# Performance work log

Hardware: AMD Instinct MI355X
Metric: run time of the kernel (lower is better)

Reference implementation:

```python
import jax, jax.numpy as jnp
import numpy as np

B, N, DIM, H, DH = 1, 2048, 1024, 16, 64


def setup_inputs() -> dict:
    key = jax.random.key(0)
    k1, k2, k3 = jax.random.split(key, 3)
    x = jax.random.normal(k1, (B, N, DIM), dtype=jnp.float32)
    # LinearNoBias(dim, 6*heads*dim_head): weight [6*H*DH, DIM]
    w_qkv = jax.random.normal(k2, (6 * H * DH, DIM), dtype=jnp.float32) * (DIM ** -0.5)
    # LinearNoBias(heads*dim_head, dim): weight [DIM, H*DH]
    w_out = jax.random.normal(k3, (DIM, H * DH), dtype=jnp.float32) * ((H * DH) ** -0.5)
    return {"x": x, "w_qkv": w_qkv, "w_out": w_out}


def reference(x, w_qkv, w_out):
    b, n, _ = x.shape
    scale = DH ** -0.5
    qkvs = x @ w_qkv.T  # [b, n, 6*H*DH]
    # rearrange 'b n (qkv h d) -> qkv b h n d'
    qkvs = qkvs.reshape(b, n, 6, H, DH).transpose(2, 0, 3, 1, 4)
    qu, ku, vu, qc, kc, vc = qkvs
    qu = qu * scale
    qc = qc * scale

    upper = jnp.triu(jnp.ones((n, n), dtype=bool), 1)  # strict upper triangle

    # term1: causal (lower-incl-diag) qc . vu
    term1 = jnp.einsum('bhid,bhjd->bhij', qc, vu)
    term1 = jnp.where(upper, 0.0, term1)

    # sigmoid lookahead term: strict-upper only
    sig = jax.nn.sigmoid(jnp.einsum('bhid,bhjd->bhij', qu, ku))
    sig = jnp.where(upper, sig, 0.0)

    Su = jnp.einsum('bhij,bhkj->bhik', term1, sig)

    Sc = jnp.einsum('bhid,bhjd->bhij', qc, kc)
    neg = -jnp.finfo(Sc.dtype).max
    Sc = jnp.where(upper, neg, Sc)

    scores = Sc - jax.nn.silu(Su)
    attn = jax.nn.softmax(scores, axis=-1)
    out = jnp.einsum('bhij,bhjd->bhid', attn, vc)  # [b,h,n,d]
    out = out.transpose(0, 2, 1, 3).reshape(b, n, H * DH)
    return out @ w_out.T
```

## Files before the change

kernel.cpp:

```cpp
#include <hip/hip_runtime.h>

using f16 = _Float16;
using half8  = __attribute__((ext_vector_type(8))) f16;
using half4v = __attribute__((ext_vector_type(4))) f16;
using float4v = __attribute__((ext_vector_type(4))) float;

#define DEV static __device__ __forceinline__

constexpr int N = 2048, DIM = 1024, H = 16, DH = 64, F6 = 6144;
constexpr int LDSH = 136;
constexpr int TS = 128 * 128;
constexpr int NTILES = 136;
constexpr int KD = 2048 * 64;

DEV int PL(int i, int k) { return i * (i + 1) / 2 + k; }
DEV int PU(int a, int b) { return a * 16 - a * (a - 1) / 2 + (b - a); }

template<int ROWS, int THREADS>
DEV void stage64(const f16* __restrict__ g, int strideHalves, f16* lds, int tid) {
#pragma unroll
  for (int q = 0; q < (ROWS * 8) / THREADS; ++q) {
    const int chunk = q * THREADS + tid;
    const int m = chunk >> 3, c = (chunk & 7) ^ (m & 7);
    const f16* gp = g + (size_t)m * strideHalves + c * 8;
    __builtin_amdgcn_global_load_lds(
        (const __attribute__((address_space(1))) unsigned int*)gp,
        (__attribute__((address_space(3))) unsigned int*)(lds + chunk * 8), 16, 0, 0);
  }
}

DEV half8 rdfrag(const f16* T, int m, int ks, int q) {
  const int c = (ks * 4 + q) ^ (m & 7);
  return *(const half8*)(T + m * 64 + c * 8);
}

DEV void wfrag(f16* T, int row, int col, f16 v) {
  T[row * 64 + ((((col >> 3) ^ (row & 7)) << 3) | (col & 7))] = v;
}

DEV void gemm64(const f16* As, const f16* Bs, int wm, int wn, int l, float4v acc[4][4]) {
  const int q = l >> 4, mm = l & 15;
#pragma unroll
  for (int ks = 0; ks < 2; ++ks) {
    half8 af[4], bf[4];
#pragma unroll
    for (int mi = 0; mi < 4; ++mi) af[mi] = rdfrag(As, wm + mm + mi * 16, ks, q);
#pragma unroll
    for (int ni = 0; ni < 4; ++ni) bf[ni] = rdfrag(Bs, wn + mm + ni * 16, ks, q);
#pragma unroll
    for (int mi = 0; mi < 4; ++mi)
#pragma unroll
      for (int ni = 0; ni < 4; ++ni)
        acc[mi][ni] = __builtin_amdgcn_mfma_f32_16x16x32_f16(af[mi], bf[ni], acc[mi][ni], 0, 0, 0);
  }
}

DEV void decode_pair(int p, int& ti, int& tk) {
  int t = (int)((sqrtf(8.f * p + 1.f) - 1.f) * 0.5f);
  while (t * (t + 1) / 2 > p) --t;
  while ((t + 1) * (t + 2) / 2 <= p) ++t;
  const int i2 = p - t * (t + 1) / 2;
  ti = (15 - t) + i2;
  tk = i2;
}

__global__ __launch_bounds__(256) void k_cast(const float* __restrict__ s, f16* __restrict__ d, int n4) {
  int i = blockIdx.x * 256 + threadIdx.x;
  if (i < n4) {
    float4 v = ((const float4*)s)[i];
    half4v h;
    h[0] = (f16)v.x; h[1] = (f16)v.y; h[2] = (f16)v.z; h[3] = (f16)v.w;
    ((half4v*)d)[i] = h;
  }
}

__global__ __launch_bounds__(256) void k_qkv(const f16* __restrict__ xh, const f16* __restrict__ wh,
                                             f16* __restrict__ quh, f16* __restrict__ kuh,
                                             f16* __restrict__ vuh, f16* __restrict__ qch,
                                             f16* __restrict__ kch, f16* __restrict__ vcT,
                                             f16* __restrict__ vuT) {
  __shared__ __align__(16) f16 lds[128 * LDSH];
  f16* As = lds; f16* Bs = lds + 128 * 64;
  const int tid = threadIdx.x, w = tid >> 6, l = tid & 63;
  const int tm = blockIdx.x * 128, tf = blockIdx.y * 128;
  const int wm = (w >> 1) * 64, wn = (w & 1) * 64;
  float4v acc[4][4] = {};
  for (int k0 = 0; k0 < DIM; k0 += 64) {
    stage64<128, 256>(xh + (size_t)tm * DIM + k0, DIM, As, tid);
    stage64<128, 256>(wh + (size_t)tf * DIM + k0, DIM, Bs, tid);
    __syncthreads();
    gemm64(As, Bs, wm, wn, l, acc);
    __syncthreads();
  }
  const int rbase = (l >> 4) * 4, cidx = l & 15;
  const int t = tf >> 10;
  const float sc = (t == 0 || t == 3) ? 0.125f : 1.f;
  if (t == 5 || t == 2) {
    f16* T = (t == 5) ? vcT : vuT;
#pragma unroll
    for (int mi = 0; mi < 4; ++mi)
#pragma unroll
      for (int ni = 0; ni < 4; ++ni) {
        const int f = tf + wn + ni * 16 + cidx;
        const int h = (f & 1023) >> 6, d = f & 63;
        half4v p;
#pragma unroll
        for (int r = 0; r < 4; ++r) p[r] = (f16)acc[mi][ni][r];
        *(half4v*)(T + ((size_t)h * DH + d) * N + (tm + wm + mi * 16 + rbase)) = p;
      }
  }
  if (t != 5) {
#pragma unroll
    for (int mi = 0; mi < 4; ++mi)
#pragma unroll
      for (int ni = 0; ni < 4; ++ni)
#pragma unroll
        for (int r = 0; r < 4; ++r)
          lds[(wm + mi * 16 + rbase + r) * LDSH + wn + ni * 16 + cidx] = (f16)(acc[mi][ni][r] * sc);
    __syncthreads();
    f16* dst = (t == 0) ? quh : (t == 1) ? kuh : (t == 2) ? vuh : (t == 3) ? qch : kch;
    const int hb = (tf & 1023) >> 6;
#pragma unroll
    for (int q = 0; q < 8; ++q) {
      const int idx = q * 256 + tid, row = idx >> 4, c = idx & 15;
      const int h = hb + (c >> 3), d0 = (c & 7) * 8, n = tm + row;
      *(half8*)(dst + ((size_t)h * N + n) * DH + d0) = *(const half8*)(lds + row * LDSH + c * 8);
    }
  }
}

__global__ __launch_bounds__(256) void k_dsig(const f16* __restrict__ quh, const f16* __restrict__ kuh,
                                              const f16* __restrict__ qch, const f16* __restrict__ vuh,
                                              const f16* __restrict__ vuT,
                                              f16* __restrict__ sigb, f16* __restrict__ DC,
                                              f16* __restrict__ diagb, int h0) {
  __shared__ __align__(16) f16 L[32768];
  f16* quA = L; f16* kuB = L + 8192; f16* s1 = L + 16384; f16* s2 = L + 24576;
  int b, a;
  decode_pair(blockIdx.y, b, a);
  const int hl = blockIdx.x, h = h0 + hl;
  const int tid = threadIdx.x, w = tid >> 6, l = tid & 63;
  const int q = l >> 4, m = l & 15;
  const int wm = (w >> 1) * 64, wn = (w & 1) * 64;
  const size_t ho = (size_t)h * N * DH;

  stage64<128, 256>(quh + ho + (size_t)(a * 128) * DH, DH, quA, tid);
  stage64<128, 256>(kuh + ho + (size_t)(b * 128) * DH, DH, kuB, tid);
  __syncthreads();
  float4v acc[4][4] = {};
  gemm64(quA, kuB, wm, wn, l, acc);
  __syncthreads();
  stage64<64, 256>(vuT + (size_t)h * DH * N + b * 128, N, kuB, tid);
  stage64<64, 256>(vuT + (size_t)h * DH * N + b * 128 + 64, N, kuB + 4096, tid);
#pragma unroll
  for (int mi = 0; mi < 4; ++mi)
#pragma unroll
    for (int ni = 0; ni < 4; ++ni)
#pragma unroll
      for (int r = 0; r < 4; ++r) {
        const int row = wm + mi * 16 + q * 4 + r;
        const int col = wn + ni * 16 + m;
        const float x = acc[mi][ni][r];
        const f16 sv = (b * 128 + col > a * 128 + row) ? (f16)(1.f / (1.f + __expf(-x))) : (f16)0.f;
        wfrag((col < 64) ? s1 : s2, row, col & 63, sv);
      }
  __syncthreads();
  {
    f16* Sg = sigb + ((size_t)hl * NTILES + PU(a, b)) * TS;
#pragma unroll
    for (int qq = 0; qq < 8; ++qq) {
      const int idx = qq * 256 + tid, row = idx >> 4, c = idx & 15;
      const f16* p = ((c >> 3) ? s2 : s1) + row * 64 + (((c & 7) ^ (row & 7)) << 3);
      *(half8*)(Sg + (size_t)row * 128 + c * 8) = *(const half8*)p;
    }
  }
  float4v dacc[2][4] = {};
#pragma unroll
  for (int p = 0; p < 2; ++p)
#pragma unroll
    for (int ks = 0; ks < 2; ++ks) {
      half8 bf[4], af[2];
#pragma unroll
      for (int ni = 0; ni < 4; ++ni) bf[ni] = rdfrag(kuB + p * 4096, ni * 16 + m, ks, q);
#pragma unroll
      for (int mi = 0; mi < 2; ++mi) af[mi] = rdfrag(p ? s2 : s1, w * 32 + mi * 16 + m, ks, q);
#pragma unroll
      for (int mi = 0; mi < 2; ++mi)
#pragma unroll
        for (int ni = 0; ni < 4; ++ni)
          dacc[mi][ni] = __builtin_amdgcn_mfma_f32_16x16x32_f16(af[mi], bf[ni], dacc[mi][ni], 0, 0, 0);
    }
  __syncthreads();
  if (a == b) {
    stage64<128, 256>(qch + ho + (size_t)(a * 128) * DH, DH, quA, tid);
    stage64<128, 256>(vuh + ho + (size_t)(a * 128) * DH, DH, kuB, tid);
  }
  {
    f16* epsD = s1;
#pragma unroll
    for (int mi = 0; mi < 2; ++mi)
#pragma unroll
      for (int ni = 0; ni < 4; ++ni)
#pragma unroll
        for (int r = 0; r < 4; ++r)
          epsD[(w * 32 + mi * 16 + q * 4 + r) * 68 + ni * 16 + m] = (f16)dacc[mi][ni][r];
    __syncthreads();
    f16* Dg = DC + ((size_t)hl * 16 + b) * KD + (size_t)(a * 128) * 64;
#pragma unroll
    for (int qq = 0; qq < 4; ++qq) {
      const int idx = qq * 256 + tid, row = idx >> 3, c = idx & 7;
      *(half8*)(Dg + (size_t)row * 64 + c * 8) = *(const half8*)(epsD + row * 68 + c * 8);
    }
  }
  if (a == b) {
    float4v tacc[4][4] = {};
    gemm64(quA, kuB, wm, wn, l, tacc);
    f16* Tg = diagb + ((size_t)hl * 16 + a) * TS;
#pragma unroll
    for (int mi = 0; mi < 4; ++mi)
#pragma unroll
      for (int ni = 0; ni < 4; ++ni)
#pragma unroll
        for (int r = 0; r < 4; ++r) {
          const int row = wm + mi * 16 + q * 4 + r, col = wn + ni * 16 + m;
          Tg[(size_t)row * 128 + col] = (col <= row) ? (f16)tacc[mi][ni][r] : (f16)0.f;
        }
  }
}

__global__ __launch_bounds__(256) void k_scan(f16* __restrict__ DC, int total) {
  const int idx = blockIdx.x * 256 + threadIdx.x;
  if (idx >= total) return;
  const int g = idx >> 17, off = idx & (KD - 1);
  const int a = off >> 13;
  f16* p = DC + (size_t)g * 16 * KD + off;
  float s = 0.f;
#pragma unroll
  for (int T = 0; T < 16; ++T) {
    const float v = (T >= a) ? (float)p[(size_t)T * KD] : 0.f;
    p[(size_t)T * KD] = (f16)s;
    s += v;
  }
}

__global__ __launch_bounds__(256) void k_favs(const f16* __restrict__ qch, const f16* __restrict__ kch,
                                              const f16* __restrict__ DC, const f16* __restrict__ sigb,
                                              const f16* __restrict__ diagb, const f16* __restrict__ vcT,
                                              f16* __restrict__ Oh, int h0) {
  __shared__ float mlds[4][32], llds[4][32];
  __shared__ __align__(16) float olds[32][68];
  __shared__ __align__(16) f16 plds[4][32 * 64];
  const int hl = blockIdx.x, h = h0 + hl;
  const int mt = 63 - (int)blockIdx.y;
  const int tid = threadIdx.x, w = tid >> 6, l = tid & 63;
  const int q = l >> 4, m = l & 15;
  const int ti = mt >> 2, r0 = mt * 32;
  const size_t ho = (size_t)h * N * DH;
  const f16* qc = qch + ho;
  const f16* kc = kch + ho;
  const f16* Cb = DC + ((size_t)hl * 16 + ti) * KD;
  const f16* Td = diagb + ((size_t)hl * 16 + ti) * TS;
  const f16* Sgb = sigb + (size_t)hl * NTILES * TS;
  const f16* V = vcT + (size_t)h * DH * N;
  f16* pw = plds[w];

  half8 qcA[2][2], tdA[2][4];
  const int dr = (mt & 3) * 32;
#pragma unroll
  for (int mi = 0; mi < 2; ++mi) {
#pragma unroll
    for (int ks = 0; ks < 2; ++ks)
      qcA[mi][ks] = *(const half8*)(qc + (size_t)(r0 + mi * 16 + m) * DH + ks * 32 + q * 8);
#pragma unroll
    for (int ks = 0; ks < 4; ++ks)
      tdA[mi][ks] = *(const half8*)(Td + (size_t)(dr + mi * 16 + m) * 128 + ks * 32 + q * 8);
  }

  float4v o[2][4] = {};
  float mrun[2][4], lrun[2][4];
#pragma unroll
  for (int mi = 0; mi < 2; ++mi)
#pragma unroll
    for (int r = 0; r < 4; ++r) { mrun[mi][r] = -1e30f; lrun[mi][r] = 0.f; }

  const int jtmax = mt >> 1;
  for (int jt = w; jt <= jtmax; jt += 4) {
    const int k0 = jt * 64;
    const int tkt = jt >> 1, koff = (jt & 1) * 64;
    const f16* Sg = Sgb + (size_t)PU(tkt, ti) * TS;
    float4v s[2][4] = {};
#pragma unroll
    for (int ks = 0; ks < 2; ++ks) {
      half8 bf[4];
#pragma unroll
      for (int ni = 0; ni < 4; ++ni)
        bf[ni] = *(const half8*)(Cb + (size_t)(k0 + ni * 16 + m) * 64 + ks * 32 + q * 8);
#pragma unroll
      for (int mi = 0; mi < 2; ++mi)
#pragma unroll
        for (int ni = 0; ni < 4; ++ni)
          s[mi][ni] = __builtin_amdgcn_mfma_f32_16x16x32_f16(qcA[mi][ks], bf[ni], s[mi][ni], 0, 0, 0);
    }
#pragma unroll
    for (int ks = 0; ks < 4; ++ks) {
      half8 bf[4];
#pragma unroll
      for (int ni = 0; ni < 4; ++ni)
        bf[ni] = *(const half8*)(Sg + (size_t)(koff + ni * 16 + m) * 128 + ks * 32 + q * 8);
#pragma unroll
      for (int mi = 0; mi < 2; ++mi)
#pragma unroll
        for (int ni = 0; ni < 4; ++ni)
          s[mi][ni] = __builtin_amdgcn_mfma_f32_16x16x32_f16(tdA[mi][ks], bf[ni], s[mi][ni], 0, 0, 0);
    }
#pragma unroll
    for (int mi = 0; mi < 2; ++mi)
#pragma unroll
      for (int ni = 0; ni < 4; ++ni)
#pragma unroll
        for (int r = 0; r < 4; ++r) {
          const float x = s[mi][ni][r];
          s[mi][ni][r] = -(x / (1.f + __expf(-x)));
        }
#pragma unroll
    for (int ks = 0; ks < 2; ++ks) {
      half8 bf[4];
#pragma unroll
      for (int ni = 0; ni < 4; ++ni)
        bf[ni] = *(const half8*)(kc + (size_t)(k0 + ni * 16 + m) * DH + ks * 32 + q * 8);
#pragma unroll
      for (int mi = 0; mi < 2; ++mi)
#pragma unroll
        for (int ni = 0; ni < 4; ++ni)
          s[mi][ni] = __builtin_amdgcn_mfma_f32_16x16x32_f16(qcA[mi][ks], bf[ni], s[mi][ni], 0, 0, 0);
    }
    if (jt == jtmax) {
#pragma unroll
      for (int mi = 0; mi < 2; ++mi)
#pragma unroll
        for (int ni = 0; ni < 4; ++ni) {
          const int col = k0 + ni * 16 + m;
#pragma unroll
          for (int r = 0; r < 4; ++r)
            if (col > r0 + mi * 16 + q * 4 + r) s[mi][ni][r] = -1e30f;
        }
    }
    float al[2][4], ts[2][4];
#pragma unroll
    for (int mi = 0; mi < 2; ++mi)
#pragma unroll
      for (int r = 0; r < 4; ++r) {
        float tmx = fmaxf(fmaxf(s[mi][0][r], s[mi][1][r]), fmaxf(s[mi][2][r], s[mi][3][r]));
#pragma unroll
        for (int x = 1; x < 16; x <<= 1) tmx = fmaxf(tmx, __shfl_xor(tmx, x));
        const float nm = fmaxf(mrun[mi][r], tmx);
        al[mi][r] = __expf(mrun[mi][r] - nm);
        mrun[mi][r] = nm;
        ts[mi][r] = 0.f;
      }
#pragma unroll
    for (int mi = 0; mi < 2; ++mi)
#pragma unroll
      for (int ni = 0; ni < 4; ++ni)
#pragma unroll
        for (int r = 0; r < 4; ++r) {
          const float p = __expf(s[mi][ni][r] - mrun[mi][r]);
          wfrag(pw, mi * 16 + q * 4 + r, ni * 16 + m, (f16)p);
          ts[mi][r] += p;
        }
#pragma unroll
    for (int mi = 0; mi < 2; ++mi)
#pragma unroll
      for (int r = 0; r < 4; ++r) {
#pragma unroll
        for (int x = 1; x < 16; x <<= 1) ts[mi][r] += __shfl_xor(ts[mi][r], x);
        lrun[mi][r] = lrun[mi][r] * al[mi][r] + ts[mi][r];
#pragma unroll
        for (int ni = 0; ni < 4; ++ni) o[mi][ni][r] *= al[mi][r];
      }
#pragma unroll
    for (int ks = 0; ks < 2; ++ks) {
      half8 af[2], bf[4];
#pragma unroll
      for (int mi = 0; mi < 2; ++mi) af[mi] = rdfrag(pw, mi * 16 + m, ks, q);
#pragma unroll
      for (int ni = 0; ni < 4; ++ni)
        bf[ni] = *(const half8*)(V + (size_t)(ni * 16 + m) * N + k0 + ks * 32 + q * 8);
#pragma unroll
      for (int mi = 0; mi < 2; ++mi)
#pragma unroll
        for (int ni = 0; ni < 4; ++ni)
          o[mi][ni] = __builtin_amdgcn_mfma_f32_16x16x32_f16(af[mi], bf[ni], o[mi][ni], 0, 0, 0);
    }
  }
  if (m == 0)
#pragma unroll
    for (int mi = 0; mi < 2; ++mi)
#pragma unroll
      for (int r = 0; r < 4; ++r) {
        mlds[w][mi * 16 + q * 4 + r] = mrun[mi][r];
        llds[w][mi * 16 + q * 4 + r] = lrun[mi][r];
      }
  __syncthreads();
#pragma unroll
  for (int mi = 0; mi < 2; ++mi)
#pragma unroll
    for (int r = 0; r < 4; ++r) {
      const int row = mi * 16 + q * 4 + r;
      const float mstar = fmaxf(fmaxf(mlds[0][row], mlds[1][row]), fmaxf(mlds[2][row], mlds[3][row]));
      const float sw = __expf(mlds[w][row] - mstar);
#pragma unroll
      for (int ni = 0; ni < 4; ++ni) o[mi][ni][r] *= sw;
    }
#pragma unroll
  for (int t = 0; t < 4; ++t) {
    if (w == t) {
#pragma unroll
      for (int mi = 0; mi < 2; ++mi)
#pragma unroll
        for (int ni = 0; ni < 4; ++ni)
#pragma unroll
          for (int r = 0; r < 4; ++r) {
            const int row = mi * 16 + q * 4 + r, col = ni * 16 + m;
            if (t == 0) olds[row][col] = o[mi][ni][r];
            else olds[row][col] += o[mi][ni][r];
          }
    }
    __syncthreads();
  }
  const int row = tid >> 3, c = tid & 7;
  const float mstar = fmaxf(fmaxf(mlds[0][row], mlds[1][row]), fmaxf(mlds[2][row], mlds[3][row]));
  float denom = 0.f;
#pragma unroll
  for (int t = 0; t < 4; ++t) denom += __expf(mlds[t][row] - mstar) * llds[t][row];
  const float inv = 1.f / denom;
  half8 o8;
#pragma unroll
  for (int e = 0; e < 8; ++e) o8[e] = (f16)(olds[row][c * 8 + e] * inv);
  *(half8*)(Oh + (size_t)(mt * 32 + row) * (H * DH) + h * DH + c * 8) = o8;
}

__global__ __launch_bounds__(256) void k_out(const f16* __restrict__ Oh, const f16* __restrict__ wo,
                                             float* __restrict__ out) {
  __shared__ __align__(16) f16 lds[128 * LDSH];
  f16* As = lds; f16* Bs = lds + 128 * 64;
  const int tid = threadIdx.x, w = tid >> 6, l = tid & 63;
  const int tm = blockIdx.x * 128, tn = blockIdx.y * 128;
  const int wm = (w >> 1) * 64, wn = (w & 1) * 64;
  float4v acc[4][4] = {};
  for (int k0 = 0; k0 < DIM; k0 += 64) {
    stage64<128, 256>(Oh + (size_t)tm * DIM + k0, DIM, As, tid);
    stage64<128, 256>(wo + (size_t)tn * DIM + k0, DIM, Bs, tid);
    __syncthreads();
    gemm64(As, Bs, wm, wn, l, acc);
    __syncthreads();
  }
  const int rbase = (l >> 4) * 4, cidx = l & 15;
#pragma unroll
  for (int mi = 0; mi < 4; ++mi)
#pragma unroll
    for (int ni = 0; ni < 4; ++ni)
#pragma unroll
      for (int r = 0; r < 4; ++r) {
        const int n = tm + wm + mi * 16 + rbase + r;
        const int dmo = tn + wn + ni * 16 + cidx;
        out[(size_t)n * DIM + dmo] = acc[mi][ni][r];
      }
}

extern "C" void kernel_launch(void* const* d_in, const int* in_sizes, int n_in,
                              void* d_out, int out_size, void* d_ws, size_t ws_size,
                              hipStream_t stream) {
  const float* x = (const float*)d_in[0];
  const float* wqkv = (const float*)d_in[1];
  const float* wout = (const float*)d_in[2];
  float* out = (float*)d_out;
  char* ws = (char*)d_ws;

  size_t off = 0;
  auto alloc = [&](size_t b) { size_t o = off; off += (b + 255) & ~(size_t)255; return o; };
  f16* xh  = (f16*)(ws + alloc((size_t)N * DIM * 2));
  f16* wqh = (f16*)(ws + alloc((size_t)F6 * DIM * 2));
  f16* woh = (f16*)(ws + alloc((size_t)DIM * H * DH * 2));
  f16* quh = (f16*)(ws + alloc((size_t)H * N * DH * 2));
  f16* kuh = (f16*)(ws + alloc((size_t)H * N * DH * 2));
  f16* vuh = (f16*)(ws + alloc((size_t)H * N * DH * 2));
  f16* qch = (f16*)(ws + alloc((size_t)H * N * DH * 2));
  f16* kch = (f16*)(ws + alloc((size_t)H * N * DH * 2));
  f16* vcT = (f16*)(ws + alloc((size_t)H * DH * N * 2));
  f16* vuT = (f16*)(ws + alloc((size_t)H * DH * N * 2));
  f16* Oh  = (f16*)(ws + alloc((size_t)N * H * DH * 2));
  const size_t persist = off;

  const size_t per_head = ((size_t)NTILES * TS + (size_t)16 * KD + (size_t)16 * TS) * 2;
  int G = (ws_size > persist + 4096) ? (int)((ws_size - persist - 4096) / per_head) : 1;
  if (G < 1) G = 1;
  if (G > 16) G = 16;
  {
    const int R = (H + G - 1) / G;
    G = (H + R - 1) / R;
  }
  f16* sigb  = (f16*)(ws + alloc((size_t)G * NTILES * TS * 2));
  f16* DC    = (f16*)(ws + alloc((size_t)G * 16 * KD * 2));
  f16* diagb = (f16*)(ws + alloc((size_t)G * 16 * TS * 2));

  k_cast<<<(N * DIM / 4 + 255) / 256, 256, 0, stream>>>(x, xh, N * DIM / 4);
  k_cast<<<(F6 * DIM / 4 + 255) / 256, 256, 0, stream>>>(wqkv, wqh, F6 * DIM / 4);
  k_cast<<<(DIM * H * DH / 4 + 255) / 256, 256, 0, stream>>>(wout, woh, DIM * H * DH / 4);

  k_qkv<<<dim3(N / 128, F6 / 128), 256, 0, stream>>>(xh, wqh, quh, kuh, vuh, qch, kch, vcT, vuT);

  for (int h0 = 0; h0 < H; h0 += G) {
    const int Gr = (H - h0 < G) ? (H - h0) : G;
    k_dsig<<<dim3(Gr, 136), 256, 0, stream>>>(quh, kuh, qch, vuh, vuT, sigb, DC, diagb, h0);
    k_scan<<<(Gr * KD + 255) / 256, 256, 0, stream>>>(DC, Gr * KD);
    k_favs<<<dim3(Gr, 64), 256, 0, stream>>>(qch, kch, DC, sigb, diagb, vcT, Oh, h0);
  }

  k_out<<<dim3(16, 8), 256, 0, stream>>>(Oh, woh, out);
}
```

Baseline: 323.1 us.

## Prefetch B-fragments ahead of MFMAs and interleave block-row order in k_favs

The inner loop of k_favs now issues the global loads for the C, K, sigmoid and V fragments early, into registers, so that their latency overlaps earlier MFMA chains instead of stalling each k-step. The block-to-row-tile mapping also changes from strictly descending to alternating long and short causal rows, which changes how work is spread over time across CUs. This raises register pressure (about 48 extra half8 values held live), which could cut occupancy or cause spills.

```diff
diff --git a/kernel.cpp b/kernel.cpp
--- a/kernel.cpp
+++ b/kernel.cpp
@@ -251,7 +251,8 @@
   __shared__ __align__(16) float olds[32][68];
   __shared__ __align__(16) f16 plds[4][32 * 64];
   const int hl = blockIdx.x, h = h0 + hl;
-  const int mt = 63 - (int)blockIdx.y;
+  const int y = (int)blockIdx.y;
+  const int mt = (y < 32) ? (63 - 2 * y) : (2 * (y - 32));
   const int tid = threadIdx.x, w = tid >> 6, l = tid & 63;
   const int q = l >> 4, m = l & 15;
   const int ti = mt >> 2, r0 = mt * 32;
@@ -288,31 +289,56 @@
     const int k0 = jt * 64;
     const int tkt = jt >> 1, koff = (jt & 1) * 64;
     const f16* Sg = Sgb + (size_t)PU(tkt, ti) * TS;
+    half8 bC[2][4], bK[2][4], bS0[2][4];
+#pragma unroll
+    for (int ks = 0; ks < 2; ++ks)
+#pragma unroll
+      for (int ni = 0; ni < 4; ++ni)
+        bC[ks][ni] = *(const half8*)(Cb + (size_t)(k0 + ni * 16 + m) * 64 + ks * 32 + q * 8);
+#pragma unroll
+    for (int ks = 0; ks < 2; ++ks)
+#pragma unroll
+      for (int ni = 0; ni < 4; ++ni)
+        bK[ks][ni] = *(const half8*)(kc + (size_t)(k0 + ni * 16 + m) * DH + ks * 32 + q * 8);
+#pragma unroll
+    for (int ks = 0; ks < 2; ++ks)
+#pragma unroll
+      for (int ni = 0; ni < 4; ++ni)
+        bS0[ks][ni] = *(const half8*)(Sg + (size_t)(koff + ni * 16 + m) * 128 + ks * 32 + q * 8);
     float4v s[2][4] = {};
 #pragma unroll
-    for (int ks = 0; ks < 2; ++ks) {
-      half8 bf[4];
-#pragma unroll
-      for (int ni = 0; ni < 4; ++ni)
-        bf[ni] = *(const half8*)(Cb + (size_t)(k0 + ni * 16 + m) * 64 + ks * 32 + q * 8);
-#pragma unroll
-      for (int mi = 0; mi < 2; ++mi)
-#pragma unroll
-        for (int ni = 0; ni < 4; ++ni)
-          s[mi][ni] = __builtin_amdgcn_mfma_f32_16x16x32_f16(qcA[mi][ks], bf[ni], s[mi][ni], 0, 0, 0);
-    }
-#pragma unroll
-    for (int ks = 0; ks < 4; ++ks) {
-      half8 bf[4];
-#pragma unroll
-      for (int ni = 0; ni < 4; ++ni)
-        bf[ni] = *(const half8*)(Sg + (size_t)(koff + ni * 16 + m) * 128 + ks * 32 + q * 8);
-#pragma unroll
-      for (int mi = 0; mi < 2; ++mi)
-#pragma unroll
-        for (int ni = 0; ni < 4; ++ni)
-          s[mi][ni] = __builtin_amdgcn_mfma_f32_16x16x32_f16(tdA[mi][ks], bf[ni], s[mi][ni], 0, 0, 0);
-    }
+    for (int ks = 0; ks < 2; ++ks)
+#pragma unroll
+      for (int mi = 0; mi < 2; ++mi)
+#pragma unroll
+        for (int ni = 0; ni < 4; ++ni)
+          s[mi][ni] = __builtin_amdgcn_mfma_f32_16x16x32_f16(qcA[mi][ks], bC[ks][ni], s[mi][ni], 0, 0, 0);
+    half8 bS1[2][4];
+#pragma unroll
+    for (int ks = 0; ks < 2; ++ks)
+#pragma unroll
+      for (int ni = 0; ni < 4; ++ni)
+        bS1[ks][ni] = *(const half8*)(Sg + (size_t)(koff + ni * 16 + m) * 128 + (ks + 2) * 32 + q * 8);
+#pragma unroll
+    for (int ks = 0; ks < 2; ++ks)
+#pragma unroll
+      for (int mi = 0; mi < 2; ++mi)
+#pragma unroll
+        for (int ni = 0; ni < 4; ++ni)
+          s[mi][ni] = __builtin_amdgcn_mfma_f32_16x16x32_f16(tdA[mi][ks], bS0[ks][ni], s[mi][ni], 0, 0, 0);
+    half8 bV[2][4];
+#pragma unroll
+    for (int ks = 0; ks < 2; ++ks)
+#pragma unroll
+      for (int ni = 0; ni < 4; ++ni)
+        bV[ks][ni] = *(const half8*)(V + (size_t)(ni * 16 + m) * N + k0 + ks * 32 + q * 8);
+#pragma unroll
+    for (int ks = 0; ks < 2; ++ks)
+#pragma unroll
+      for (int mi = 0; mi < 2; ++mi)
+#pragma unroll
+        for (int ni = 0; ni < 4; ++ni)
+          s[mi][ni] = __builtin_amdgcn_mfma_f32_16x16x32_f16(tdA[mi][ks + 2], bS1[ks][ni], s[mi][ni], 0, 0, 0);
 #pragma unroll
     for (int mi = 0; mi < 2; ++mi)
 #pragma unroll
@@ -323,17 +349,12 @@
           s[mi][ni][r] = -(x / (1.f + __expf(-x)));
         }
 #pragma unroll
-    for (int ks = 0; ks < 2; ++ks) {
-      half8 bf[4];
-#pragma unroll
-      for (int ni = 0; ni < 4; ++ni)
-        bf[ni] = *(const half8*)(kc + (size_t)(k0 + ni * 16 + m) * DH + ks * 32 + q * 8);
-#pragma unroll
-      for (int mi = 0; mi < 2; ++mi)
-#pragma unroll
-        for (int ni = 0; ni < 4; ++ni)
-          s[mi][ni] = __builtin_amdgcn_mfma_f32_16x16x32_f16(qcA[mi][ks], bf[ni], s[mi][ni], 0, 0, 0);
-    }
+    for (int ks = 0; ks < 2; ++ks)
+#pragma unroll
+      for (int mi = 0; mi < 2; ++mi)
+#pragma unroll
+        for (int ni = 0; ni < 4; ++ni)
+          s[mi][ni] = __builtin_amdgcn_mfma_f32_16x16x32_f16(qcA[mi][ks], bK[ks][ni], s[mi][ni], 0, 0, 0);
     if (jt == jtmax) {
 #pragma unroll
       for (int mi = 0; mi < 2; ++mi)
@@ -380,17 +401,14 @@
       }
 #pragma unroll
     for (int ks = 0; ks < 2; ++ks) {
-      half8 af[2], bf[4];
+      half8 af[2];
 #pragma unroll
       for (int mi = 0; mi < 2; ++mi) af[mi] = rdfrag(pw, mi * 16 + m, ks, q);
 #pragma unroll
-      for (int ni = 0; ni < 4; ++ni)
-        bf[ni] = *(const half8*)(V + (size_t)(ni * 16 + m) * N + k0 + ks * 32 + q * 8);
-#pragma unroll
-      for (int mi = 0; mi < 2; ++mi)
-#pragma unroll
-        for (int ni = 0; ni < 4; ++ni)
-          o[mi][ni] = __builtin_amdgcn_mfma_f32_16x16x32_f16(af[mi], bf[ni], o[mi][ni], 0, 0, 0);
+      for (int mi = 0; mi < 2; ++mi)
+#pragma unroll
+        for (int ni = 0; ni < 4; ++ni)
+          o[mi][ni] = __builtin_amdgcn_mfma_f32_16x16x32_f16(af[mi], bV[ks][ni], o[mi][ni], 0, 0, 0);
     }
   }
   if (m == 0)
```

Result: slower. 338.9 us (+4.9%).

## Store kc, vcT, sigmoid tiles and DC in MFMA-fragment-packed layout

Applied to the files above, without the earlier changes.

The producer kernels now write kc, vcT, the sigmoid tiles and the DC buffer in a layout packed by MFMA B-fragment, so each lane's half8 load in k_favs sits at a contiguous offset (q*512+m*8), and a wavefront's loads become contiguous 1 KB runs instead of strided row reads. The V fragments are also loaded earlier in the loop, before the SiLU/softmax math, so their latency can overlap that compute. This aims to cut uncoalesced global/L2 traffic in the main attention loop. The cost is more complex index math in the epilogues, and the layouts are tightly coupled across three kernels.

```diff
diff --git a/kernel.cpp b/kernel.cpp
--- a/kernel.cpp
+++ b/kernel.cpp
@@ -12,6 +12,7 @@
 constexpr int TS = 128 * 128;
 constexpr int NTILES = 136;
 constexpr int KD = 2048 * 64;
+
 
 DEV int PL(int i, int k) { return i * (i + 1) / 2 + k; }
 DEV int PU(int a, int b) { return a * 16 - a * (a - 1) / 2 + (b - a); }
@@ -96,17 +97,24 @@
   const int t = tf >> 10;
   const float sc = (t == 0 || t == 3) ? 0.125f : 1.f;
   if (t == 5 || t == 2) {
-    f16* T = (t == 5) ? vcT : vuT;
 #pragma unroll
     for (int mi = 0; mi < 4; ++mi)
 #pragma unroll
       for (int ni = 0; ni < 4; ++ni) {
         const int f = tf + wn + ni * 16 + cidx;
         const int h = (f & 1023) >> 6, d = f & 63;
+        const int n = tm + wm + mi * 16 + rbase;
         half4v p;
 #pragma unroll
         for (int r = 0; r < 4; ++r) p[r] = (f16)acc[mi][ni][r];
-        *(half4v*)(T + ((size_t)h * DH + d) * N + (tm + wm + mi * 16 + rbase)) = p;
+        if (t == 5) {
+          const int ks2 = (n & 63) >> 5, q2 = (n >> 3) & 3;
+          const int inner = ks2 * 256 + q2 * 64 + (d >> 4) * 16 + (d & 15);
+          *(half4v*)(vcT + (size_t)h * DH * N + (size_t)(n >> 6) * 4096 +
+                     (size_t)inner * 8 + (n & 7)) = p;
+        } else {
+          *(half4v*)(vuT + ((size_t)h * DH + d) * N + n) = p;
+        }
       }
   }
   if (t != 5) {
@@ -118,13 +126,27 @@
         for (int r = 0; r < 4; ++r)
           lds[(wm + mi * 16 + rbase + r) * LDSH + wn + ni * 16 + cidx] = (f16)(acc[mi][ni][r] * sc);
     __syncthreads();
-    f16* dst = (t == 0) ? quh : (t == 1) ? kuh : (t == 2) ? vuh : (t == 3) ? qch : kch;
     const int hb = (tf & 1023) >> 6;
-#pragma unroll
-    for (int q = 0; q < 8; ++q) {
-      const int idx = q * 256 + tid, row = idx >> 4, c = idx & 15;
-      const int h = hb + (c >> 3), d0 = (c & 7) * 8, n = tm + row;
-      *(half8*)(dst + ((size_t)h * N + n) * DH + d0) = *(const half8*)(lds + row * LDSH + c * 8);
+    if (t == 4) {
+#pragma unroll
+      for (int qq = 0; qq < 8; ++qq) {
+        const int idx = qq * 256 + tid;
+        const int hh = idx >> 10, f = idx & 1023;
+        const int pl = f >> 9, inner = f & 511;
+        const int m2 = inner & 15, ni2 = (inner >> 4) & 3, q2 = (inner >> 6) & 3, ks2 = inner >> 8;
+        const int row = pl * 64 + ni2 * 16 + m2;
+        const int col = hh * 64 + ks2 * 32 + q2 * 8;
+        *(half8*)(kch + (size_t)(hb + hh) * N * DH + ((size_t)(tm >> 6) + pl) * 4096 +
+                  (size_t)inner * 8) = *(const half8*)(lds + row * LDSH + col);
+      }
+    } else {
+      f16* dst = (t == 0) ? quh : (t == 1) ? kuh : (t == 2) ? vuh : qch;
+#pragma unroll
+      for (int q = 0; q < 8; ++q) {
+        const int idx = q * 256 + tid, row = idx >> 4, c = idx & 15;
+        const int h = hb + (c >> 3), d0 = (c & 7) * 8, n = tm + row;
+        *(half8*)(dst + ((size_t)h * N + n) * DH + d0) = *(const half8*)(lds + row * LDSH + c * 8);
+      }
     }
   }
 }
@@ -169,9 +191,13 @@
     f16* Sg = sigb + ((size_t)hl * NTILES + PU(a, b)) * TS;
 #pragma unroll
     for (int qq = 0; qq < 8; ++qq) {
-      const int idx = qq * 256 + tid, row = idx >> 4, c = idx & 15;
-      const f16* p = ((c >> 3) ? s2 : s1) + row * 64 + (((c & 7) ^ (row & 7)) << 3);
-      *(half8*)(Sg + (size_t)row * 128 + c * 8) = *(const half8*)p;
+      const int idx = qq * 256 + tid;
+      const int hf = idx >> 10, inner = idx & 1023;
+      const int m2 = inner & 15, ni2 = (inner >> 4) & 3, q2 = (inner >> 6) & 3, ks2 = inner >> 8;
+      const int row = hf * 64 + ni2 * 16 + m2;
+      const int c8 = ks2 * 4 + q2;
+      const f16* p = ((c8 >> 3) ? s2 : s1) + row * 64 + (((c8 & 7) ^ (row & 7)) << 3);
+      *(half8*)(Sg + (size_t)idx * 8) = *(const half8*)p;
     }
   }
   float4v dacc[2][4] = {};
@@ -205,11 +231,15 @@
         for (int r = 0; r < 4; ++r)
           epsD[(w * 32 + mi * 16 + q * 4 + r) * 68 + ni * 16 + m] = (f16)dacc[mi][ni][r];
     __syncthreads();
-    f16* Dg = DC + ((size_t)hl * 16 + b) * KD + (size_t)(a * 128) * 64;
+    f16* Dg = DC + ((size_t)hl * 16 + b) * KD + (size_t)a * 8192;
 #pragma unroll
     for (int qq = 0; qq < 4; ++qq) {
-      const int idx = qq * 256 + tid, row = idx >> 3, c = idx & 7;
-      *(half8*)(Dg + (size_t)row * 64 + c * 8) = *(const half8*)(epsD + row * 68 + c * 8);
+      const int idx = qq * 256 + tid;
+      const int pl = idx >> 9, inner = idx & 511;
+      const int m2 = inner & 15, ni2 = (inner >> 4) & 3, q2 = (inner >> 6) & 3, ks2 = inner >> 8;
+      const int row = pl * 64 + ni2 * 16 + m2;
+      const int c = ks2 * 4 + q2;
+      *(half8*)(Dg + (size_t)idx * 8) = *(const half8*)(epsD + row * 68 + c * 8);
     }
   }
   if (a == b) {
@@ -257,12 +287,13 @@
   const int ti = mt >> 2, r0 = mt * 32;
   const size_t ho = (size_t)h * N * DH;
   const f16* qc = qch + ho;
-  const f16* kc = kch + ho;
+  const f16* kcb = kch + ho;
   const f16* Cb = DC + ((size_t)hl * 16 + ti) * KD;
   const f16* Td = diagb + ((size_t)hl * 16 + ti) * TS;
   const f16* Sgb = sigb + (size_t)hl * NTILES * TS;
   const f16* V = vcT + (size_t)h * DH * N;
   f16* pw = plds[w];
+  const int lo = q * 512 + m * 8;
 
   half8 qcA[2][2], tdA[2][4];
   const int dr = (mt & 3) * 32;
@@ -285,16 +316,17 @@
 
   const int jtmax = mt >> 1;
   for (int jt = w; jt <= jtmax; jt += 4) {
-    const int k0 = jt * 64;
-    const int tkt = jt >> 1, koff = (jt & 1) * 64;
-    const f16* Sg = Sgb + (size_t)PU(tkt, ti) * TS;
+    const int tkt = jt >> 1;
+    const f16* Cp = Cb + (size_t)jt * 4096 + lo;
+    const f16* Kp = kcb + (size_t)jt * 4096 + lo;
+    const f16* Sp = Sgb + (size_t)PU(tkt, ti) * TS + (size_t)(jt & 1) * 8192 + lo;
+    const f16* Vp = V + (size_t)jt * 4096 + lo;
     float4v s[2][4] = {};
 #pragma unroll
     for (int ks = 0; ks < 2; ++ks) {
       half8 bf[4];
 #pragma unroll
-      for (int ni = 0; ni < 4; ++ni)
-        bf[ni] = *(const half8*)(Cb + (size_t)(k0 + ni * 16 + m) * 64 + ks * 32 + q * 8);
+      for (int ni = 0; ni < 4; ++ni) bf[ni] = *(const half8*)(Cp + ks * 2048 + ni * 128);
 #pragma unroll
       for (int mi = 0; mi < 2; ++mi)
 #pragma unroll
@@ -305,14 +337,18 @@
     for (int ks = 0; ks < 4; ++ks) {
       half8 bf[4];
 #pragma unroll
-      for (int ni = 0; ni < 4; ++ni)
-        bf[ni] = *(const half8*)(Sg + (size_t)(koff + ni * 16 + m) * 128 + ks * 32 + q * 8);
+      for (int ni = 0; ni < 4; ++ni) bf[ni] = *(const half8*)(Sp + ks * 2048 + ni * 128);
 #pragma unroll
       for (int mi = 0; mi < 2; ++mi)
 #pragma unroll
         for (int ni = 0; ni < 4; ++ni)
           s[mi][ni] = __builtin_amdgcn_mfma_f32_16x16x32_f16(tdA[mi][ks], bf[ni], s[mi][ni], 0, 0, 0);
     }
+    half8 bV[2][4];
+#pragma unroll
+    for (int ks = 0; ks < 2; ++ks)
+#pragma unroll
+      for (int ni = 0; ni < 4; ++ni) bV[ks][ni] = *(const half8*)(Vp + ks * 2048 + ni * 128);
 #pragma unroll
     for (int mi = 0; mi < 2; ++mi)
 #pragma unroll
@@ -326,8 +362,7 @@
     for (int ks = 0; ks < 2; ++ks) {
       half8 bf[4];
 #pragma unroll
-      for (int ni = 0; ni < 4; ++ni)
-        bf[ni] = *(const half8*)(kc + (size_t)(k0 + ni * 16 + m) * DH + ks * 32 + q * 8);
+      for (int ni = 0; ni < 4; ++ni) bf[ni] = *(const half8*)(Kp + ks * 2048 + ni * 128);
 #pragma unroll
       for (int mi = 0; mi < 2; ++mi)
 #pragma unroll
@@ -335,6 +370,7 @@
           s[mi][ni] = __builtin_amdgcn_mfma_f32_16x16x32_f16(qcA[mi][ks], bf[ni], s[mi][ni], 0, 0, 0);
     }
     if (jt == jtmax) {
+      const int k0 = jt * 64;
 #pragma unroll
       for (int mi = 0; mi < 2; ++mi)
 #pragma unroll
@@ -380,17 +416,14 @@
       }
 #pragma unroll
     for (int ks = 0; ks < 2; ++ks) {
-      half8 af[2], bf[4];
+      half8 af[2];
 #pragma unroll
       for (int mi = 0; mi < 2; ++mi) af[mi] = rdfrag(pw, mi * 16 + m, ks, q);
 #pragma unroll
-      for (int ni = 0; ni < 4; ++ni)
-        bf[ni] = *(const half8*)(V + (size_t)(ni * 16 + m) * N + k0 + ks * 32 + q * 8);
-#pragma unroll
       for (int mi = 0; mi < 2; ++mi)
 #pragma unroll
         for (int ni = 0; ni < 4; ++ni)
-          o[mi][ni] = __builtin_amdgcn_mfma_f32_16x16x32_f16(af[mi], bf[ni], o[mi][ni], 0, 0, 0);
+          o[mi][ni] = __builtin_amdgcn_mfma_f32_16x16x32_f16(af[mi], bV[ks][ni], o[mi][ni], 0, 0, 0);
     }
   }
   if (m == 0)
```

Measured after the change: 296.8 us. 8.1% less time.
